# Performance work log

Hardware: AMD Instinct MI355X
Metric: run time of the kernel (lower is better)

Reference implementation:

```python
import math
import jax, jax.numpy as jnp
import numpy as np

EMBED_SIZE = 1024
NUM_HEADS = 16
HEAD_DIM = EMBED_SIZE // NUM_HEADS
N, L = 8, 1024
MASK_FILL = -1e3  # value used by masked_fill in the original (NOT -inf)
SCALE = 1.0 / math.sqrt(EMBED_SIZE)  # original divides by embed_size**0.5, not head_dim


def setup_inputs() -> dict:
    key = jax.random.key(0)
    ks = jax.random.split(key, 7)
    values = jax.random.normal(ks[0], (N, L, EMBED_SIZE), dtype=jnp.float32)
    keys_t = jax.random.normal(ks[1], (N, L, EMBED_SIZE), dtype=jnp.float32)
    queries = jax.random.normal(ks[2], (N, L, EMBED_SIZE), dtype=jnp.float32)
    attn_mask = jax.random.randint(ks[3], (1, 1, L, L), 0, 2, dtype=jnp.int32)
    scr_key_padding_mask = jax.random.randint(ks[4], (N, 1, 1, L), 0, 2, dtype=jnp.int32)
    # fc_out: nn.Linear(embed_size, embed_size) with bias
    fc_w = jax.random.normal(ks[5], (EMBED_SIZE, EMBED_SIZE), dtype=jnp.float32) * (1.0 / math.sqrt(EMBED_SIZE))
    fc_b = jax.random.normal(ks[6], (EMBED_SIZE,), dtype=jnp.float32) * 0.01
    return {"values": values, "keys": keys_t, "queries": queries,
            "fc_w": fc_w, "fc_b": fc_b,
            "attn_mask": attn_mask, "scr_key_padding_mask": scr_key_padding_mask}


def reference(values, keys, queries, fc_w, fc_b, attn_mask, scr_key_padding_mask):
    n, q_len, e = queries.shape
    k_len = keys.shape[1]
    h, d = NUM_HEADS, HEAD_DIM
    # NOTE: the original defines per-head Linear projections but never applies them
    v = values.reshape(n, k_len, h, d)
    k = keys.reshape(n, k_len, h, d)
    q = queries.reshape(n, q_len, h, d)
    energy = jnp.einsum('nqhd,nkhd->nhqk', q, k)  # [n, h, q, k]
    am = attn_mask[:, :, :k_len, :k_len]
    energy = jnp.where(am == 0, MASK_FILL, energy)
    energy = jnp.where(scr_key_padding_mask == 0, MASK_FILL, energy)
    attention = jax.nn.softmax(energy * SCALE, axis=3)
    out = jnp.einsum('nhql,nlhd->nqhd', attention, v).reshape(n, q_len, h * d)
    return out @ fc_w.T + fc_b
```

## Files before the change

kernel.cpp:

```cpp
#include <hip/hip_runtime.h>

#define L_SEQ 1024
#define EMB 1024
#define NH 16
#define HD 64

typedef _Float16 half8 __attribute__((ext_vector_type(8)));
typedef _Float16 half4v __attribute__((ext_vector_type(4)));
typedef __fp16 h2 __attribute__((ext_vector_type(2)));
typedef float f32x4 __attribute__((ext_vector_type(4)));
typedef float f32x16 __attribute__((ext_vector_type(16)));
typedef float fvec4 __attribute__((ext_vector_type(4)));
typedef unsigned int u32;
typedef u32 u32x4 __attribute__((ext_vector_type(4)));
typedef unsigned long long u64;

constexpr float C2 = 0.045084220027780106f;

constexpr int PP = 66;

__device__ __forceinline__ void async16(const void* g, void* l) {
    __builtin_amdgcn_global_load_lds((const __attribute__((address_space(1))) u32*)g,
                                     (__attribute__((address_space(3))) u32*)l, 16, 0, 0);
}

__global__ void prep_kernel(const int* __restrict__ am, u32* __restrict__ bits,
                            const int* __restrict__ pad, u32* __restrict__ pbits,
                            const float* __restrict__ w, _Float16* __restrict__ o) {
    const int b = blockIdx.x;
    const int i = b * 256 + threadIdx.x;
    const int lane = threadIdx.x & 63;
    u64 bal = __ballot(am[i] != 0);
    if (lane == 0)       bits[i >> 5] = (u32)bal;
    else if (lane == 32) bits[i >> 5] = (u32)(bal >> 32);
    if (b < 32) {
        u64 pb = __ballot(pad[i] != 0);
        if (lane == 0)       pbits[i >> 5] = (u32)pb;
        else if (lane == 32) pbits[i >> 5] = (u32)(pb >> 32);
    }
    if (b < 1024) {
        size_t j = (size_t)i * 4;
        fvec4 v = *(const fvec4*)(w + j);
        half4v hh;
#pragma unroll
        for (int k = 0; k < 4; ++k) hh[k] = (_Float16)v[k];
        *(half4v*)(o + j) = hh;
    }
}

__global__ __launch_bounds__(256) void cvt_kv_kernel(
    const float* __restrict__ keys, const float* __restrict__ values,
    _Float16* __restrict__ K16, _Float16* __restrict__ Vt16)
{
    __shared__ __align__(16) _Float16 Vt[64 * PP];
    const int tid = threadIdx.x;
    const int kt = blockIdx.x, h = blockIdx.y, n = blockIdx.z;
    const int kbase = kt * 64;
    const int r = tid >> 2, c0 = (tid & 3) * 16;
    const int nh = n * NH + h;

    {
        const float* src = keys + ((size_t)(n * L_SEQ + kbase + r)) * EMB + h * HD + c0;
        fvec4 a0 = *(const fvec4*)(src),     a1 = *(const fvec4*)(src + 4);
        fvec4 a2 = *(const fvec4*)(src + 8), a3 = *(const fvec4*)(src + 12);
        half8 o0, o1;
#pragma unroll
        for (int j = 0; j < 4; ++j) {
            o0[j] = (_Float16)(a0[j] * C2); o0[j + 4] = (_Float16)(a1[j] * C2);
            o1[j] = (_Float16)(a2[j] * C2); o1[j + 4] = (_Float16)(a3[j] * C2);
        }
        _Float16* dst = K16 + ((size_t)nh * L_SEQ + kbase + r) * HD + c0;
        *(half8*)dst = o0; *(half8*)(dst + 8) = o1;
    }
    {
        const float* src = values + ((size_t)(n * L_SEQ + kbase + r)) * EMB + h * HD + c0;
        fvec4 vv[4];
        vv[0] = *(const fvec4*)(src);     vv[1] = *(const fvec4*)(src + 4);
        vv[2] = *(const fvec4*)(src + 8); vv[3] = *(const fvec4*)(src + 12);
#pragma unroll
        for (int i = 0; i < 16; ++i)
            Vt[(c0 + i) * PP + r] = (_Float16)vv[i >> 2][i & 3];
    }
    __syncthreads();
    {
        const int d = tid >> 2, k0 = (tid & 3) * 16;
        const u32* vr = (const u32*)((const char*)Vt + (size_t)d * (PP * 2) + 2 * k0);
        u32 a[8];
#pragma unroll
        for (int m = 0; m < 8; ++m) a[m] = vr[m];
        u32x4 lo = {a[0], a[1], a[2], a[3]};
        u32x4 hi2 = {a[4], a[5], a[6], a[7]};
        _Float16* dst = Vt16 + ((size_t)nh * HD + d) * L_SEQ + kbase + k0;
        *(half8*)dst = __builtin_bit_cast(half8, lo);
        *(half8*)(dst + 8) = __builtin_bit_cast(half8, hi2);
    }
}

__global__ __launch_bounds__(256, 3) void attn_kernel(
    const _Float16* __restrict__ K16, const _Float16* __restrict__ Vt16,
    const float* __restrict__ queries, const u32* __restrict__ mbits,
    const u32* __restrict__ pbits, _Float16* __restrict__ out_f16)
{
    __shared__ __align__(16) _Float16 K_lds[2][64 * 64];
    __shared__ __align__(16) _Float16 V_lds[2][64 * 64];
    __shared__ __align__(8)  u32 mtab[32];

    const int tid  = threadIdx.x;
    const int lane = tid & 63;
    const int wv   = tid >> 6;
    const int l32  = lane & 31;
    const int hi   = lane >> 5;
    const int bid  = blockIdx.x;
    const int nh = bid & 127, qt = bid >> 7;
    const int n = nh >> 4, h = nh & 15;
    const int qbase = qt * 128;
    const int q = qbase + wv * 32 + l32;
    const int rsw = l32 & 7;

    const _Float16* Kt_base = K16 + (size_t)nh * L_SEQ * HD;
    const _Float16* Vt_base = Vt16 + (size_t)nh * HD * L_SEQ;
    const int gch = (lane & 7) ^ ((lane >> 3) & 7);

    auto stage = [&](int buf, int kt) {
        const int kbase = kt * 64;
#pragma unroll
        for (int s2 = 0; s2 < 2; ++s2) {
            const int row = wv * 16 + s2 * 8 + (lane >> 3);
            async16(Kt_base + (size_t)(kbase + row) * HD + gch * 8,
                    &K_lds[buf][(wv * 16 + s2 * 8) * 64]);
            async16(Vt_base + (size_t)row * L_SEQ + kbase + gch * 8,
                    &V_lds[buf][(wv * 16 + s2 * 8) * 64]);
        }
    };

    uint2 wm_cur = *(const uint2*)(&mbits[(size_t)q * 32]);
    u32 pl_cur = pbits[n << 5];
    u32 ph_cur = pbits[(n << 5) + 1];
    stage(0, 0);

    if (tid < 16) {
        mtab[tid * 2]     = ((tid & 1) ? 0x3C00u : 0u) | ((tid & 2) ? 0x3C000000u : 0u);
        mtab[tid * 2 + 1] = ((tid & 4) ? 0x3C00u : 0u) | ((tid & 8) ? 0x3C000000u : 0u);
    }

    half8 qf[4];
    {
        const float* qp = queries + ((size_t)(n * L_SEQ + q)) * EMB + h * HD;
#pragma unroll
        for (int c = 0; c < 4; ++c) {
            fvec4 a = *(const fvec4*)(qp + c * 16 + hi * 8);
            fvec4 b = *(const fvec4*)(qp + c * 16 + hi * 8 + 4);
#pragma unroll
            for (int j = 0; j < 4; ++j) { qf[c][j] = (_Float16)a[j]; qf[c][j + 4] = (_Float16)b[j]; }
        }
    }

    f32x16 Ov[2];
#pragma unroll
    for (int dt = 0; dt < 2; ++dt)
#pragma unroll
        for (int r = 0; r < 16; ++r) Ov[dt][r] = 0.f;
    float lsum = 0.f;
    const h2 one2 = {(__fp16)1.f, (__fp16)1.f};

    int cur = 0;
#pragma unroll 2
    for (int kt = 0; kt < L_SEQ / 64; ++kt) {
        __syncthreads();

        uint2 wm_next = {0u, 0u};
        u32 pl_next = 0u, ph_next = 0u;
        if (kt + 1 < L_SEQ / 64) {
            wm_next = *(const uint2*)(&mbits[(size_t)q * 32 + (kt + 1) * 2]);
            pl_next = pbits[(n << 5) + ((kt + 1) << 1)];
            ph_next = pbits[(n << 5) + ((kt + 1) << 1) + 1];
            stage(cur ^ 1, kt + 1);
        }

        u32 w[2];
        w[0] = wm_cur.x & pl_cur;
        w[1] = wm_cur.y & ph_cur;

        f32x16 St[2];
#pragma unroll
        for (int i = 0; i < 2; ++i)
#pragma unroll
            for (int r = 0; r < 16; ++r) St[i][r] = 0.f;

        const _Float16* kb = &K_lds[cur][0];
#pragma unroll
        for (int c = 0; c < 4; ++c) {
            const int ch = ((2 * c + hi) ^ rsw) * 8;
            half8 kf0 = *(const half8*)(kb + l32 * 64 + ch);
            half8 kf1 = *(const half8*)(kb + (32 + l32) * 64 + ch);
            St[0] = __builtin_amdgcn_mfma_f32_32x32x16_f16(kf0, qf[c], St[0], 0, 0, 0);
            St[1] = __builtin_amdgcn_mfma_f32_32x32x16_f16(kf1, qf[c], St[1], 0, 0, 0);
        }

        u32 pa[4][4];
#pragma unroll
        for (int i = 0; i < 2; ++i) {
#pragma unroll
            for (int rgp = 0; rgp < 2; ++rgp) {
                const int rg_a = 2 * rgp, rg_b = 2 * rgp + 1;
                const u32 m4a = (w[i] >> (8 * rg_a + 4 * hi)) & 15u;
                const u32 m4b = (w[i] >> (8 * rg_b + 4 * hi)) & 15u;
                const uint2 mma = *(const uint2*)(&mtab[m4a * 2]);
                const uint2 mmb = *(const uint2*)(&mtab[m4b * 2]);
                const float pa0 = __builtin_amdgcn_exp2f(St[i][4 * rg_a + 0]);
                const float pa1 = __builtin_amdgcn_exp2f(St[i][4 * rg_a + 1]);
                const float pa2 = __builtin_amdgcn_exp2f(St[i][4 * rg_a + 2]);
                const float pa3 = __builtin_amdgcn_exp2f(St[i][4 * rg_a + 3]);
                const float pb0 = __builtin_amdgcn_exp2f(St[i][4 * rg_b + 0]);
                const float pb1 = __builtin_amdgcn_exp2f(St[i][4 * rg_b + 1]);
                const float pb2 = __builtin_amdgcn_exp2f(St[i][4 * rg_b + 2]);
                const float pb3 = __builtin_amdgcn_exp2f(St[i][4 * rg_b + 3]);
                const h2 a0 = __builtin_amdgcn_cvt_pkrtz(pa0, pa1) * __builtin_bit_cast(h2, mma.x);
                const h2 a1 = __builtin_amdgcn_cvt_pkrtz(pa2, pa3) * __builtin_bit_cast(h2, mma.y);
                const h2 b0 = __builtin_amdgcn_cvt_pkrtz(pb0, pb1) * __builtin_bit_cast(h2, mmb.x);
                const h2 b1 = __builtin_amdgcn_cvt_pkrtz(pb2, pb3) * __builtin_bit_cast(h2, mmb.y);
                lsum = __builtin_amdgcn_fdot2(a0, one2, lsum, false);
                lsum = __builtin_amdgcn_fdot2(a1, one2, lsum, false);
                lsum = __builtin_amdgcn_fdot2(b0, one2, lsum, false);
                lsum = __builtin_amdgcn_fdot2(b1, one2, lsum, false);
                u32 A0 = __builtin_bit_cast(u32, a0), A1 = __builtin_bit_cast(u32, a1);
                u32 B0 = __builtin_bit_cast(u32, b0), B1 = __builtin_bit_cast(u32, b1);
                asm("v_permlane32_swap_b32 %0, %1" : "+v"(A0), "+v"(B0));
                asm("v_permlane32_swap_b32 %0, %1" : "+v"(A1), "+v"(B1));
                const int ks = i * 2 + rgp;
                pa[ks][0] = A0; pa[ks][1] = A1; pa[ks][2] = B0; pa[ks][3] = B1;
            }
        }

        const _Float16* vb = &V_lds[cur][0];
#pragma unroll
        for (int ks = 0; ks < 4; ++ks) {
            u32x4 pw = {pa[ks][0], pa[ks][1], pa[ks][2], pa[ks][3]};
            half8 pB = __builtin_bit_cast(half8, pw);
            const int ch = ((2 * ks + hi) ^ rsw) * 8;
            half8 vf0 = *(const half8*)(vb + l32 * 64 + ch);
            half8 vf1 = *(const half8*)(vb + (32 + l32) * 64 + ch);
            Ov[0] = __builtin_amdgcn_mfma_f32_32x32x16_f16(pB, vf0, Ov[0], 0, 0, 0);
            Ov[1] = __builtin_amdgcn_mfma_f32_32x32x16_f16(pB, vf1, Ov[1], 0, 0, 0);
        }

        wm_cur = wm_next; pl_cur = pl_next; ph_cur = ph_next;
        cur ^= 1;
    }

    lsum += __shfl_xor(lsum, 32);
    float linv[16];
#pragma unroll
    for (int reg = 0; reg < 16; ++reg) {
        const int qrel = (reg & 3) + 8 * (reg >> 2) + 4 * hi;
        linv[reg] = 1.0f / fmaxf(__shfl(lsum, qrel), 1e-25f);
    }
#pragma unroll
    for (int reg = 0; reg < 16; ++reg) {
        const int qrow = qbase + wv * 32 + (reg & 3) + 8 * (reg >> 2) + 4 * hi;
        _Float16* op = out_f16 + ((size_t)(n * L_SEQ + qrow)) * EMB + h * HD;
        op[l32]      = (_Float16)(Ov[0][reg] * linv[reg]);
        op[32 + l32] = (_Float16)(Ov[1][reg] * linv[reg]);
    }
}

__global__ __launch_bounds__(256) void fc_kernel(
    const _Float16* __restrict__ A, const _Float16* __restrict__ W,
    const float* __restrict__ bias, float* __restrict__ C)
{
    __shared__ __align__(16) _Float16 As[2][128 * 64];
    __shared__ __align__(16) _Float16 Ws[2][128 * 64];

    const int tid = threadIdx.x;
    const int lane = tid & 63;
    const int wv = tid >> 6;
    const int l16 = lane & 15;
    const int quad = lane >> 4;
    const int wm = (wv >> 1) * 64, wn = (wv & 1) * 64;
    const int Mb = blockIdx.x * 128, Nb = blockIdx.y * 128;
    const int xr = l16 & 7;

    auto stage = [&](int buf, int k0) {
#pragma unroll
        for (int s = 0; s < 4; ++s) {
            const int row = wv * 32 + s * 8 + (lane >> 3);
            const int sc = (lane & 7) ^ (row & 7);
            async16(A + (size_t)(Mb + row) * EMB + k0 + sc * 8, &As[buf][(wv * 32 + s * 8) * 64]);
            async16(W + (size_t)(Nb + row) * EMB + k0 + sc * 8, &Ws[buf][(wv * 32 + s * 8) * 64]);
        }
    };

    f32x4 acc[4][4];
#pragma unroll
    for (int i = 0; i < 4; ++i)
#pragma unroll
        for (int j = 0; j < 4; ++j) acc[i][j] = (f32x4){0.f, 0.f, 0.f, 0.f};

    stage(0, 0);
    int cur = 0;
#pragma unroll 2
    for (int k0 = 0; k0 < EMB; k0 += 64) {
        __syncthreads();
        if (k0 + 64 < EMB) stage(cur ^ 1, k0 + 64);

        half8 af[4][2], bf[4][2];
#pragma unroll
        for (int i = 0; i < 4; ++i)
#pragma unroll
            for (int kk = 0; kk < 2; ++kk) {
                const int ch = (((kk * 4 + quad) ^ xr)) * 8;
                af[i][kk] = *(const half8*)(&As[cur][(wm + i * 16 + l16) * 64 + ch]);
                bf[i][kk] = *(const half8*)(&Ws[cur][(wn + i * 16 + l16) * 64 + ch]);
            }
#pragma unroll
        for (int i = 0; i < 4; ++i)
#pragma unroll
            for (int j = 0; j < 4; ++j)
#pragma unroll
                for (int kk = 0; kk < 2; ++kk)
                    acc[i][j] = __builtin_amdgcn_mfma_f32_16x16x32_f16(af[i][kk], bf[j][kk], acc[i][j], 0, 0, 0);
        cur ^= 1;
    }

#pragma unroll
    for (int i = 0; i < 4; ++i) {
        const int m = Mb + wm + i * 16 + quad * 4;
#pragma unroll
        for (int j = 0; j < 4; ++j) {
            const int jc = Nb + wn + j * 16 + l16;
            const float b = bias[jc];
#pragma unroll
            for (int reg = 0; reg < 4; ++reg)
                C[(size_t)(m + reg) * EMB + jc] = acc[i][j][reg] + b;
        }
    }
}

extern "C" void kernel_launch(void* const* d_in, const int* in_sizes, int n_in,
                              void* d_out, int out_size, void* d_ws, size_t ws_size,
                              hipStream_t stream) {
    const float* values  = (const float*)d_in[0];
    const float* keys    = (const float*)d_in[1];
    const float* queries = (const float*)d_in[2];
    const float* fc_w    = (const float*)d_in[3];
    const float* fc_b    = (const float*)d_in[4];
    const int*   amask   = (const int*)d_in[5];
    const int*   pmask   = (const int*)d_in[6];
    float* out = (float*)d_out;

    char* w = (char*)d_ws;
    _Float16* attn_out = (_Float16*)w;
    _Float16* w_f16    = (_Float16*)(w + (size_t)16 * 1024 * 1024);
    u32*      mbits    = (u32*)(w + (size_t)18 * 1024 * 1024);
    u32*      pbits    = (u32*)(w + (size_t)18 * 1024 * 1024 + 128 * 1024);
    _Float16* K16      = (_Float16*)(w + (size_t)19 * 1024 * 1024);
    _Float16* Vt16     = (_Float16*)(w + (size_t)35 * 1024 * 1024);

    prep_kernel<<<4096, 256, 0, stream>>>(amask, mbits, pmask, pbits, fc_w, w_f16);
    cvt_kv_kernel<<<dim3(16, 16, 8), 256, 0, stream>>>(keys, values, K16, Vt16);
    attn_kernel<<<1024, 256, 0, stream>>>(K16, Vt16, queries, mbits, pbits, attn_out);
    fc_kernel<<<dim3(64, 8), 256, 0, stream>>>(attn_out, w_f16, fc_b, out);
}
```

Before: 223.6 us.

## Process two 32-query tiles per wave to reuse K/V LDS fragments

Each wave now handles 64 queries as two 32-row tiles (A and B) that share each K and V fragment read from LDS, so a block covers 256 queries and the grid is halved to 512 blocks. This halves LDS traffic and global K/V staging per query and interleaves S/P computation per 32-key half to limit live registers. The cost is more VGPRs (four O accumulators plus two Q fragment sets), so the occupancy hint drops from 3 to 2 blocks per CU. With only 512 blocks on a 256-CU device, load balance and latency hiding may also suffer.

```diff
diff --git a/kernel.cpp b/kernel.cpp
--- a/kernel.cpp
+++ b/kernel.cpp
@@ -96,7 +96,7 @@
     }
 }
 
-__global__ __launch_bounds__(256, 3) void attn_kernel(
+__global__ __launch_bounds__(256, 2) void attn_kernel(
     const _Float16* __restrict__ K16, const _Float16* __restrict__ Vt16,
     const float* __restrict__ queries, const u32* __restrict__ mbits,
     const u32* __restrict__ pbits, _Float16* __restrict__ out_f16)
@@ -113,8 +113,8 @@
     const int bid  = blockIdx.x;
     const int nh = bid & 127, qt = bid >> 7;
     const int n = nh >> 4, h = nh & 15;
-    const int qbase = qt * 128;
-    const int q = qbase + wv * 32 + l32;
+    const int qbase = qt * 256;
+    const int qA = qbase + wv * 64 + l32;
     const int rsw = l32 & 7;
 
     const _Float16* Kt_base = K16 + (size_t)nh * L_SEQ * HD;
@@ -133,9 +133,10 @@
         }
     };
 
-    uint2 wm_cur = *(const uint2*)(&mbits[(size_t)q * 32]);
-    u32 pl_cur = pbits[n << 5];
-    u32 ph_cur = pbits[(n << 5) + 1];
+    uint2 wmA = *(const uint2*)(&mbits[(size_t)qA * 32]);
+    uint2 wmB = *(const uint2*)(&mbits[(size_t)(qA + 32) * 32]);
+    u32 pl = pbits[n << 5];
+    u32 ph = pbits[(n << 5) + 1];
     stage(0, 0);
 
     if (tid < 16) {
@@ -143,24 +144,28 @@
         mtab[tid * 2 + 1] = ((tid & 4) ? 0x3C00u : 0u) | ((tid & 8) ? 0x3C000000u : 0u);
     }
 
-    half8 qf[4];
+    half8 qfA[4], qfB[4];
     {
-        const float* qp = queries + ((size_t)(n * L_SEQ + q)) * EMB + h * HD;
+        const float* qpA = queries + ((size_t)(n * L_SEQ + qA)) * EMB + h * HD;
+        const float* qpB = qpA + (size_t)32 * EMB;
 #pragma unroll
         for (int c = 0; c < 4; ++c) {
-            fvec4 a = *(const fvec4*)(qp + c * 16 + hi * 8);
-            fvec4 b = *(const fvec4*)(qp + c * 16 + hi * 8 + 4);
-#pragma unroll
-            for (int j = 0; j < 4; ++j) { qf[c][j] = (_Float16)a[j]; qf[c][j + 4] = (_Float16)b[j]; }
-        }
-    }
-
-    f32x16 Ov[2];
-#pragma unroll
-    for (int dt = 0; dt < 2; ++dt)
-#pragma unroll
-        for (int r = 0; r < 16; ++r) Ov[dt][r] = 0.f;
-    float lsum = 0.f;
+            fvec4 a = *(const fvec4*)(qpA + c * 16 + hi * 8);
+            fvec4 b = *(const fvec4*)(qpA + c * 16 + hi * 8 + 4);
+            fvec4 e = *(const fvec4*)(qpB + c * 16 + hi * 8);
+            fvec4 f = *(const fvec4*)(qpB + c * 16 + hi * 8 + 4);
+#pragma unroll
+            for (int j = 0; j < 4; ++j) {
+                qfA[c][j] = (_Float16)a[j]; qfA[c][j + 4] = (_Float16)b[j];
+                qfB[c][j] = (_Float16)e[j]; qfB[c][j + 4] = (_Float16)f[j];
+            }
+        }
+    }
+
+    f32x16 OvA0, OvA1, OvB0, OvB1;
+#pragma unroll
+    for (int r = 0; r < 16; ++r) { OvA0[r] = 0.f; OvA1[r] = 0.f; OvB0[r] = 0.f; OvB1[r] = 0.f; }
+    float lsA = 0.f, lsB = 0.f;
     const h2 one2 = {(__fp16)1.f, (__fp16)1.f};
 
     int cur = 0;
@@ -168,99 +173,131 @@
     for (int kt = 0; kt < L_SEQ / 64; ++kt) {
         __syncthreads();
 
-        uint2 wm_next = {0u, 0u};
-        u32 pl_next = 0u, ph_next = 0u;
+        uint2 wmA_n = {0u, 0u}, wmB_n = {0u, 0u};
+        u32 pl_n = 0u, ph_n = 0u;
         if (kt + 1 < L_SEQ / 64) {
-            wm_next = *(const uint2*)(&mbits[(size_t)q * 32 + (kt + 1) * 2]);
-            pl_next = pbits[(n << 5) + ((kt + 1) << 1)];
-            ph_next = pbits[(n << 5) + ((kt + 1) << 1) + 1];
+            wmA_n = *(const uint2*)(&mbits[(size_t)qA * 32 + (kt + 1) * 2]);
+            wmB_n = *(const uint2*)(&mbits[(size_t)(qA + 32) * 32 + (kt + 1) * 2]);
+            pl_n = pbits[(n << 5) + ((kt + 1) << 1)];
+            ph_n = pbits[(n << 5) + ((kt + 1) << 1) + 1];
             stage(cur ^ 1, kt + 1);
         }
 
-        u32 w[2];
-        w[0] = wm_cur.x & pl_cur;
-        w[1] = wm_cur.y & ph_cur;
-
-        f32x16 St[2];
-#pragma unroll
-        for (int i = 0; i < 2; ++i)
-#pragma unroll
-            for (int r = 0; r < 16; ++r) St[i][r] = 0.f;
+        const u32 wA[2] = {wmA.x & pl, wmA.y & ph};
+        const u32 wB[2] = {wmB.x & pl, wmB.y & ph};
 
         const _Float16* kb = &K_lds[cur][0];
-#pragma unroll
-        for (int c = 0; c < 4; ++c) {
-            const int ch = ((2 * c + hi) ^ rsw) * 8;
-            half8 kf0 = *(const half8*)(kb + l32 * 64 + ch);
-            half8 kf1 = *(const half8*)(kb + (32 + l32) * 64 + ch);
-            St[0] = __builtin_amdgcn_mfma_f32_32x32x16_f16(kf0, qf[c], St[0], 0, 0, 0);
-            St[1] = __builtin_amdgcn_mfma_f32_32x32x16_f16(kf1, qf[c], St[1], 0, 0, 0);
-        }
-
-        u32 pa[4][4];
+        const _Float16* vb = &V_lds[cur][0];
+
 #pragma unroll
         for (int i = 0; i < 2; ++i) {
+            f32x16 StA, StB;
+#pragma unroll
+            for (int r = 0; r < 16; ++r) { StA[r] = 0.f; StB[r] = 0.f; }
+#pragma unroll
+            for (int c = 0; c < 4; ++c) {
+                const int ch = ((2 * c + hi) ^ rsw) * 8;
+                half8 kf = *(const half8*)(kb + (i * 32 + l32) * 64 + ch);
+                StA = __builtin_amdgcn_mfma_f32_32x32x16_f16(kf, qfA[c], StA, 0, 0, 0);
+                StB = __builtin_amdgcn_mfma_f32_32x32x16_f16(kf, qfB[c], StB, 0, 0, 0);
+            }
+
+            u32 paA[2][4], paB[2][4];
 #pragma unroll
             for (int rgp = 0; rgp < 2; ++rgp) {
                 const int rg_a = 2 * rgp, rg_b = 2 * rgp + 1;
-                const u32 m4a = (w[i] >> (8 * rg_a + 4 * hi)) & 15u;
-                const u32 m4b = (w[i] >> (8 * rg_b + 4 * hi)) & 15u;
-                const uint2 mma = *(const uint2*)(&mtab[m4a * 2]);
-                const uint2 mmb = *(const uint2*)(&mtab[m4b * 2]);
-                const float pa0 = __builtin_amdgcn_exp2f(St[i][4 * rg_a + 0]);
-                const float pa1 = __builtin_amdgcn_exp2f(St[i][4 * rg_a + 1]);
-                const float pa2 = __builtin_amdgcn_exp2f(St[i][4 * rg_a + 2]);
-                const float pa3 = __builtin_amdgcn_exp2f(St[i][4 * rg_a + 3]);
-                const float pb0 = __builtin_amdgcn_exp2f(St[i][4 * rg_b + 0]);
-                const float pb1 = __builtin_amdgcn_exp2f(St[i][4 * rg_b + 1]);
-                const float pb2 = __builtin_amdgcn_exp2f(St[i][4 * rg_b + 2]);
-                const float pb3 = __builtin_amdgcn_exp2f(St[i][4 * rg_b + 3]);
-                const h2 a0 = __builtin_amdgcn_cvt_pkrtz(pa0, pa1) * __builtin_bit_cast(h2, mma.x);
-                const h2 a1 = __builtin_amdgcn_cvt_pkrtz(pa2, pa3) * __builtin_bit_cast(h2, mma.y);
-                const h2 b0 = __builtin_amdgcn_cvt_pkrtz(pb0, pb1) * __builtin_bit_cast(h2, mmb.x);
-                const h2 b1 = __builtin_amdgcn_cvt_pkrtz(pb2, pb3) * __builtin_bit_cast(h2, mmb.y);
-                lsum = __builtin_amdgcn_fdot2(a0, one2, lsum, false);
-                lsum = __builtin_amdgcn_fdot2(a1, one2, lsum, false);
-                lsum = __builtin_amdgcn_fdot2(b0, one2, lsum, false);
-                lsum = __builtin_amdgcn_fdot2(b1, one2, lsum, false);
-                u32 A0 = __builtin_bit_cast(u32, a0), A1 = __builtin_bit_cast(u32, a1);
-                u32 B0 = __builtin_bit_cast(u32, b0), B1 = __builtin_bit_cast(u32, b1);
-                asm("v_permlane32_swap_b32 %0, %1" : "+v"(A0), "+v"(B0));
-                asm("v_permlane32_swap_b32 %0, %1" : "+v"(A1), "+v"(B1));
+                const int sh_a = 8 * rg_a + 4 * hi, sh_b = 8 * rg_b + 4 * hi;
+                {
+                    const u32 m4a = (wA[i] >> sh_a) & 15u;
+                    const u32 m4b = (wA[i] >> sh_b) & 15u;
+                    const uint2 mma = *(const uint2*)(&mtab[m4a * 2]);
+                    const uint2 mmb = *(const uint2*)(&mtab[m4b * 2]);
+                    const float p0 = __builtin_amdgcn_exp2f(StA[4 * rg_a + 0]);
+                    const float p1 = __builtin_amdgcn_exp2f(StA[4 * rg_a + 1]);
+                    const float p2 = __builtin_amdgcn_exp2f(StA[4 * rg_a + 2]);
+                    const float p3 = __builtin_amdgcn_exp2f(StA[4 * rg_a + 3]);
+                    const float p4 = __builtin_amdgcn_exp2f(StA[4 * rg_b + 0]);
+                    const float p5 = __builtin_amdgcn_exp2f(StA[4 * rg_b + 1]);
+                    const float p6 = __builtin_amdgcn_exp2f(StA[4 * rg_b + 2]);
+                    const float p7 = __builtin_amdgcn_exp2f(StA[4 * rg_b + 3]);
+                    const h2 a0 = __builtin_amdgcn_cvt_pkrtz(p0, p1) * __builtin_bit_cast(h2, mma.x);
+                    const h2 a1 = __builtin_amdgcn_cvt_pkrtz(p2, p3) * __builtin_bit_cast(h2, mma.y);
+                    const h2 b0 = __builtin_amdgcn_cvt_pkrtz(p4, p5) * __builtin_bit_cast(h2, mmb.x);
+                    const h2 b1 = __builtin_amdgcn_cvt_pkrtz(p6, p7) * __builtin_bit_cast(h2, mmb.y);
+                    lsA = __builtin_amdgcn_fdot2(a0, one2, lsA, false);
+                    lsA = __builtin_amdgcn_fdot2(a1, one2, lsA, false);
+                    lsA = __builtin_amdgcn_fdot2(b0, one2, lsA, false);
+                    lsA = __builtin_amdgcn_fdot2(b1, one2, lsA, false);
+                    u32 A0 = __builtin_bit_cast(u32, a0), A1 = __builtin_bit_cast(u32, a1);
+                    u32 B0 = __builtin_bit_cast(u32, b0), B1 = __builtin_bit_cast(u32, b1);
+                    asm("v_permlane32_swap_b32 %0, %1" : "+v"(A0), "+v"(B0));
+                    asm("v_permlane32_swap_b32 %0, %1" : "+v"(A1), "+v"(B1));
+                    paA[rgp][0] = A0; paA[rgp][1] = A1; paA[rgp][2] = B0; paA[rgp][3] = B1;
+                }
+                {
+                    const u32 m4a = (wB[i] >> sh_a) & 15u;
+                    const u32 m4b = (wB[i] >> sh_b) & 15u;
+                    const uint2 mma = *(const uint2*)(&mtab[m4a * 2]);
+                    const uint2 mmb = *(const uint2*)(&mtab[m4b * 2]);
+                    const float p0 = __builtin_amdgcn_exp2f(StB[4 * rg_a + 0]);
+                    const float p1 = __builtin_amdgcn_exp2f(StB[4 * rg_a + 1]);
+                    const float p2 = __builtin_amdgcn_exp2f(StB[4 * rg_a + 2]);
+                    const float p3 = __builtin_amdgcn_exp2f(StB[4 * rg_a + 3]);
+                    const float p4 = __builtin_amdgcn_exp2f(StB[4 * rg_b + 0]);
+                    const float p5 = __builtin_amdgcn_exp2f(StB[4 * rg_b + 1]);
+                    const float p6 = __builtin_amdgcn_exp2f(StB[4 * rg_b + 2]);
+                    const float p7 = __builtin_amdgcn_exp2f(StB[4 * rg_b + 3]);
+                    const h2 a0 = __builtin_amdgcn_cvt_pkrtz(p0, p1) * __builtin_bit_cast(h2, mma.x);
+                    const h2 a1 = __builtin_amdgcn_cvt_pkrtz(p2, p3) * __builtin_bit_cast(h2, mma.y);
+                    const h2 b0 = __builtin_amdgcn_cvt_pkrtz(p4, p5) * __builtin_bit_cast(h2, mmb.x);
+                    const h2 b1 = __builtin_amdgcn_cvt_pkrtz(p6, p7) * __builtin_bit_cast(h2, mmb.y);
+                    lsB = __builtin_amdgcn_fdot2(a0, one2, lsB, false);
+                    lsB = __builtin_amdgcn_fdot2(a1, one2, lsB, false);
+                    lsB = __builtin_amdgcn_fdot2(b0, one2, lsB, false);
+                    lsB = __builtin_amdgcn_fdot2(b1, one2, lsB, false);
+                    u32 A0 = __builtin_bit_cast(u32, a0), A1 = __builtin_bit_cast(u32, a1);
+                    u32 B0 = __builtin_bit_cast(u32, b0), B1 = __builtin_bit_cast(u32, b1);
+                    asm("v_permlane32_swap_b32 %0, %1" : "+v"(A0), "+v"(B0));
+                    asm("v_permlane32_swap_b32 %0, %1" : "+v"(A1), "+v"(B1));
+                    paB[rgp][0] = A0; paB[rgp][1] = A1; paB[rgp][2] = B0; paB[rgp][3] = B1;
+                }
+            }
+
+#pragma unroll
+            for (int rgp = 0; rgp < 2; ++rgp) {
                 const int ks = i * 2 + rgp;
-                pa[ks][0] = A0; pa[ks][1] = A1; pa[ks][2] = B0; pa[ks][3] = B1;
+                const int ch = ((2 * ks + hi) ^ rsw) * 8;
+                half8 vf0 = *(const half8*)(vb + l32 * 64 + ch);
+                half8 vf1 = *(const half8*)(vb + (32 + l32) * 64 + ch);
+                u32x4 pwA = {paA[rgp][0], paA[rgp][1], paA[rgp][2], paA[rgp][3]};
+                u32x4 pwB = {paB[rgp][0], paB[rgp][1], paB[rgp][2], paB[rgp][3]};
+                half8 pA = __builtin_bit_cast(half8, pwA);
+                half8 pB = __builtin_bit_cast(half8, pwB);
+                OvA0 = __builtin_amdgcn_mfma_f32_32x32x16_f16(pA, vf0, OvA0, 0, 0, 0);
+                OvA1 = __builtin_amdgcn_mfma_f32_32x32x16_f16(pA, vf1, OvA1, 0, 0, 0);
+                OvB0 = __builtin_amdgcn_mfma_f32_32x32x16_f16(pB, vf0, OvB0, 0, 0, 0);
+                OvB1 = __builtin_amdgcn_mfma_f32_32x32x16_f16(pB, vf1, OvB1, 0, 0, 0);
             }
         }
 
-        const _Float16* vb = &V_lds[cur][0];
-#pragma unroll
-        for (int ks = 0; ks < 4; ++ks) {
-            u32x4 pw = {pa[ks][0], pa[ks][1], pa[ks][2], pa[ks][3]};
-            half8 pB = __builtin_bit_cast(half8, pw);
-            const int ch = ((2 * ks + hi) ^ rsw) * 8;
-            half8 vf0 = *(const half8*)(vb + l32 * 64 + ch);
-            half8 vf1 = *(const half8*)(vb + (32 + l32) * 64 + ch);
-            Ov[0] = __builtin_amdgcn_mfma_f32_32x32x16_f16(pB, vf0, Ov[0], 0, 0, 0);
-            Ov[1] = __builtin_amdgcn_mfma_f32_32x32x16_f16(pB, vf1, Ov[1], 0, 0, 0);
-        }
-
-        wm_cur = wm_next; pl_cur = pl_next; ph_cur = ph_next;
+        wmA = wmA_n; wmB = wmB_n; pl = pl_n; ph = ph_n;
         cur ^= 1;
     }
 
-    lsum += __shfl_xor(lsum, 32);
-    float linv[16];
+    lsA += __shfl_xor(lsA, 32);
+    lsB += __shfl_xor(lsB, 32);
 #pragma unroll
     for (int reg = 0; reg < 16; ++reg) {
         const int qrel = (reg & 3) + 8 * (reg >> 2) + 4 * hi;
-        linv[reg] = 1.0f / fmaxf(__shfl(lsum, qrel), 1e-25f);
-    }
-#pragma unroll
-    for (int reg = 0; reg < 16; ++reg) {
-        const int qrow = qbase + wv * 32 + (reg & 3) + 8 * (reg >> 2) + 4 * hi;
-        _Float16* op = out_f16 + ((size_t)(n * L_SEQ + qrow)) * EMB + h * HD;
-        op[l32]      = (_Float16)(Ov[0][reg] * linv[reg]);
-        op[32 + l32] = (_Float16)(Ov[1][reg] * linv[reg]);
+        const float liA = 1.0f / fmaxf(__shfl(lsA, qrel), 1e-25f);
+        const float liB = 1.0f / fmaxf(__shfl(lsB, qrel), 1e-25f);
+        const int qrowA = qbase + wv * 64 + qrel;
+        _Float16* opA = out_f16 + ((size_t)(n * L_SEQ + qrowA)) * EMB + h * HD;
+        _Float16* opB = opA + (size_t)32 * EMB;
+        opA[l32]      = (_Float16)(OvA0[reg] * liA);
+        opA[32 + l32] = (_Float16)(OvA1[reg] * liA);
+        opB[l32]      = (_Float16)(OvB0[reg] * liB);
+        opB[32 + l32] = (_Float16)(OvB1[reg] * liB);
     }
 }
 
@@ -358,6 +395,6 @@
 
     prep_kernel<<<4096, 256, 0, stream>>>(amask, mbits, pmask, pbits, fc_w, w_f16);
     cvt_kv_kernel<<<dim3(16, 16, 8), 256, 0, stream>>>(keys, values, K16, Vt16);
-    attn_kernel<<<1024, 256, 0, stream>>>(K16, Vt16, queries, mbits, pbits, attn_out);
+    attn_kernel<<<512, 256, 0, stream>>>(K16, Vt16, queries, mbits, pbits, attn_out);
     fc_kernel<<<dim3(64, 8), 256, 0, stream>>>(attn_out, w_f16, fc_b, out);
 }
```

Result: no change. 223.0 us (-0.3%).
